# Performance work log

Measured on AMD Instinct MI355X. Metric: run time of the kernel, lower is better.

Reference implementation:

```python
import jax, jax.numpy as jnp
import numpy as np

N0, N1, N2 = 100000, 20000, 4000
DEG = 10
G_NODES = 200000
D, ED, CD, FF, NHEAD = 512, 256, 300, 2048, 2


def _layernorm(x, g, b, eps=1e-5):
    m = jnp.mean(x, -1, keepdims=True)
    v = jnp.var(x, -1, keepdims=True)
    return (x - m) * jax.lax.rsqrt(v + eps) * g + b


def _mha(q_in, kv_in, w_in, b_in, w_out, b_out):
    # torch nn.MultiheadAttention, inputs are (seq, batch, d)
    d = q_in.shape[-1]
    wq, wk, wv = w_in[:d], w_in[d:2 * d], w_in[2 * d:]
    bq, bk, bv = b_in[:d], b_in[d:2 * d], b_in[2 * d:]
    dh = d // NHEAD
    q = (q_in @ wq.T + bq).reshape(q_in.shape[0], q_in.shape[1], NHEAD, dh)
    k = (kv_in @ wk.T + bk).reshape(kv_in.shape[0], kv_in.shape[1], NHEAD, dh)
    v = (kv_in @ wv.T + bv).reshape(kv_in.shape[0], kv_in.shape[1], NHEAD, dh)
    scores = jnp.einsum('qnhd,knhd->nhqk', q, k) * (dh ** -0.5)
    o = jnp.einsum('nhqk,knhd->qnhd', jax.nn.softmax(scores, -1), v)
    o = o.reshape(q_in.shape[0], q_in.shape[1], d)
    return o @ w_out.T + b_out


def setup_inputs() -> dict:
    key = jax.random.key(0)
    k = lambda i: jax.random.fold_in(key, i)
    inp = {}
    inp['nid0'] = jax.random.randint(k(0), (N0,), 0, G_NODES, dtype=jnp.int32)
    inp['nid1'] = jax.random.randint(k(1), (N1,), 0, G_NODES, dtype=jnp.int32)
    inp['nid2'] = jax.random.randint(k(2), (N2,), 0, G_NODES, dtype=jnp.int32)
    inp['esrc0'] = jax.random.randint(k(3), (N1 * DEG,), 0, N0, dtype=jnp.int32)
    inp['edst0'] = jnp.repeat(jnp.arange(N1, dtype=jnp.int32), DEG)
    inp['esrc1'] = jax.random.randint(k(4), (N2 * DEG,), 0, N1, dtype=jnp.int32)
    inp['edst1'] = jnp.repeat(jnp.arange(N2, dtype=jnp.int32), DEG)
    inp['content0'] = jax.random.normal(k(5), (N0, CD), jnp.float32)
    inp['content1'] = jax.random.normal(k(6), (N1, CD), jnp.float32)
    inp['content2'] = jax.random.normal(k(7), (N2, CD), jnp.float32)
    inp['node_emb_w'] = jax.random.normal(k(8), (G_NODES + 1, ED), jnp.float32) / ED
    inp['ee_w'] = jax.random.normal(k(9), (D, ED), jnp.float32) * 0.06
    inp['ee_b'] = jax.random.normal(k(10), (D,), jnp.float32) * 0.001
    inp['proj_w'] = jax.random.normal(k(11), (D, CD), jnp.float32) * 0.06
    inp['proj_b'] = jax.random.normal(k(12), (D,), jnp.float32) * 0.001
    inp['proj_g'] = jnp.ones((D,), jnp.float32)
    inp['proj_beta'] = jnp.zeros((D,), jnp.float32)
    L = 2  # decoder layers
    inp['sa_in_w'] = jax.random.normal(k(13), (L, 3 * D, D), jnp.float32) * 0.04
    inp['sa_in_b'] = jnp.zeros((L, 3 * D), jnp.float32)
    inp['sa_out_w'] = jax.random.normal(k(14), (L, D, D), jnp.float32) * 0.04
    inp['sa_out_b'] = jnp.zeros((L, D), jnp.float32)
    inp['ca_in_w'] = jax.random.normal(k(15), (L, 3 * D, D), jnp.float32) * 0.04
    inp['ca_in_b'] = jnp.zeros((L, 3 * D), jnp.float32)
    inp['ca_out_w'] = jax.random.normal(k(16), (L, D, D), jnp.float32) * 0.04
    inp['ca_out_b'] = jnp.zeros((L, D), jnp.float32)
    inp['lin1_w'] = jax.random.normal(k(17), (L, FF, D), jnp.float32) * 0.03
    inp['lin1_b'] = jnp.zeros((L, FF), jnp.float32)
    inp['lin2_w'] = jax.random.normal(k(18), (L, D, FF), jnp.float32) * 0.03
    inp['lin2_b'] = jnp.zeros((L, D), jnp.float32)
    for n in ('n1', 'n2', 'n3'):
        inp[n + '_g'] = jnp.ones((L, D), jnp.float32)
        inp[n + '_b'] = jnp.zeros((L, D), jnp.float32)
    return inp


def _forward(nid0, nid1, nid2, esrc0, edst0, esrc1, edst1,
             content0, content1, content2, node_emb_w, ee_w, ee_b,
             proj_w, proj_b, proj_g, proj_beta,
             sa_in_w, sa_in_b, sa_out_w, sa_out_b,
             ca_in_w, ca_in_b, ca_out_w, ca_out_b,
             lin1_w, lin1_b, lin2_w, lin2_b,
             n1_g, n1_b, n2_g, n2_b, n3_g, n3_b):
    def node_h(nid, content):
        nh = node_emb_w[nid + 1] @ ee_w.T + ee_b           # emb_expand(node_emb(nid+1))
        c = _layernorm(jax.nn.leaky_relu(content @ proj_w.T + proj_b, 0.1), proj_g, proj_beta)
        h = nh + c                                          # mix_embeddings (c[:, :D] == c)
        return h / jnp.maximum(jnp.linalg.norm(h, axis=1, keepdims=True), 1e-5)

    h0 = node_h(nid0, content0)
    h1 = node_h(nid1, content1)
    h2 = node_h(nid2, content2)

    def agg_mean(h_src, src, dst, n_dst):
        s = jax.ops.segment_sum(h_src[src], dst, num_segments=n_dst)
        w = jax.ops.segment_sum(jnp.ones(src.shape[0], h_src.dtype), dst, num_segments=n_dst)
        return s / w[:, None]

    # block 0: non-prediction GraphConv -> concat(mean_agg, h), L2 normalize
    m1 = agg_mean(h0, esrc0, edst0, N1)
    h1 = jnp.concatenate([m1, h1], axis=1)                  # (N1, 2D)
    h1 = h1 / jnp.maximum(jnp.linalg.norm(h1, axis=1, keepdims=True), 1e-5)

    # block 1: prediction GraphConv -> transformer-decoder fusion
    m2 = agg_mean(h1, esrc1, edst1, N2)                     # (N2, 2D)
    mem = m2.reshape(N2, 2, D).transpose(1, 0, 2)           # (n_layer=2, N2, D)
    tgt = h2[None]                                          # (1, N2, D)
    for l in range(2):  # post-norm TransformerDecoderLayer, gelu, dropout=0
        t2 = _mha(tgt, tgt, sa_in_w[l], sa_in_b[l], sa_out_w[l], sa_out_b[l])
        tgt = _layernorm(tgt + t2, n1_g[l], n1_b[l])
        t2 = _mha(tgt, mem, ca_in_w[l], ca_in_b[l], ca_out_w[l], ca_out_b[l])
        tgt = _layernorm(tgt + t2, n2_g[l], n2_b[l])
        ff = jax.nn.gelu(tgt @ lin1_w[l].T + lin1_b[l], approximate=False) @ lin2_w[l].T + lin2_b[l]
        tgt = _layernorm(tgt + ff, n3_g[l], n3_b[l])
    out = tgt[0]                                            # squeeze -> (N2, D)
    return out / jnp.maximum(jnp.linalg.norm(out, axis=1, keepdims=True), 1e-5)


def reference(nid0, nid1, nid2, esrc0, edst0, esrc1, edst1,
              content0, content1, content2, node_emb_w, ee_w, ee_b,
              proj_w, proj_b, proj_g, proj_beta,
              sa_in_w, sa_in_b, sa_out_w, sa_out_b,
              ca_in_w, ca_in_b, ca_out_w, ca_out_b,
              lin1_w, lin1_b, lin2_w, lin2_b,
              n1_g, n1_b, n2_g, n2_b, n3_g, n3_b):
    return _forward(nid0, nid1, nid2, esrc0, edst0, esrc1, edst1,
                    content0, content1, content2, node_emb_w, ee_w, ee_b,
                    proj_w, proj_b, proj_g, proj_beta,
                    sa_in_w, sa_in_b, sa_out_w, sa_out_b,
                    ca_in_w, ca_in_b, ca_out_w, ca_out_b,
                    lin1_w, lin1_b, lin2_w, lin2_b,
                    n1_g, n1_b, n2_g, n2_b, n3_g, n3_b)
```

## Files before the change

kernel.cpp:

```cpp
#include <hip/hip_runtime.h>
#include <math.h>

static constexpr int kN0  = 100000;
static constexpr int kN1  = 20000;
static constexpr int kN2  = 4000;
static constexpr int kDeg = 10;
static constexpr int kD   = 512;
static constexpr int kFF  = 2048;
static constexpr int kRows  = 48;
static constexpr int kRowsN = 32;
static constexpr int kLdA  = 584;
static constexpr int kLdG  = 520;

using short8  = __attribute__((ext_vector_type(8))) short;
using floatx4 = __attribute__((ext_vector_type(4))) float;

__device__ inline unsigned short f2bf(float f) {
    union { float f; unsigned u; } v; v.f = f;
    unsigned r = v.u + 0x7FFFu + ((v.u >> 16) & 1u);
    return (unsigned short)(r >> 16);
}

__global__ __launch_bounds__(256) void pack_node_w_kernel(
    const float* __restrict__ ee_w, const float* __restrict__ proj_w,
    ushort* __restrict__ Bp)
{
    int tid  = blockIdx.x * 256 + threadIdx.x;
    int lane = tid & 63;
    int tile = tid >> 6;
    int n     = (tile & 31) * 16 + (lane & 15);
    int kbase = (tile >> 5) * 32 + (lane >> 4) * 8;
    ushort v[8];
    #pragma unroll
    for (int j = 0; j < 8; ++j) {
        int k = kbase + j;
        float f = 0.f;
        if (k < 256)      f = ee_w[(size_t)n * 256 + k];
        else if (k < 556) f = proj_w[(size_t)n * 300 + (k - 256)];
        v[j] = f2bf(f);
    }
    uint4 u;
    u.x = (unsigned)v[0] | ((unsigned)v[1] << 16);
    u.y = (unsigned)v[2] | ((unsigned)v[3] << 16);
    u.z = (unsigned)v[4] | ((unsigned)v[5] << 16);
    u.w = (unsigned)v[6] | ((unsigned)v[7] << 16);
    *(uint4*)(Bp + (size_t)tid * 8) = u;
}

__global__ __launch_bounds__(256) void pack512_many_kernel(
    const float* __restrict__ sa_in_w, const float* __restrict__ sa_out_w,
    const float* __restrict__ ca_in_w, const float* __restrict__ ca_out_w,
    ushort* __restrict__ dst)
{
    int y = blockIdx.y, l = y / 6, m = y % 6;
    const float* W;
    switch (m) {
        case 0: W = sa_in_w  + (size_t)l * 3 * kD * kD + (size_t)2 * kD * kD; break;
        case 1: W = sa_out_w + (size_t)l * kD * kD; break;
        case 2: W = ca_in_w  + (size_t)l * 3 * kD * kD; break;
        case 3: W = ca_in_w  + (size_t)l * 3 * kD * kD + (size_t)kD * kD; break;
        case 4: W = ca_in_w  + (size_t)l * 3 * kD * kD + (size_t)2 * kD * kD; break;
        default:W = ca_out_w + (size_t)l * kD * kD; break;
    }
    int tid  = blockIdx.x * 256 + threadIdx.x;
    int lane = tid & 63;
    int tile = tid >> 6;
    int n  = (tile & 31) * 16 + (lane & 15);
    int kb = (tile >> 5) * 32 + (lane >> 4) * 8;
    const float* src = W + (size_t)n * 512 + kb;
    ushort v[8];
    #pragma unroll
    for (int j = 0; j < 8; ++j) v[j] = f2bf(src[j]);
    uint4 u;
    u.x = (unsigned)v[0] | ((unsigned)v[1] << 16);
    u.y = (unsigned)v[2] | ((unsigned)v[3] << 16);
    u.z = (unsigned)v[4] | ((unsigned)v[5] << 16);
    u.w = (unsigned)v[6] | ((unsigned)v[7] << 16);
    *(uint4*)(dst + (size_t)y * 262144 + (size_t)tid * 8) = u;
}

__global__ __launch_bounds__(256) void pack_generic_kernel(
    const float* __restrict__ src, size_t srcStride,
    ushort* __restrict__ dst, size_t dstStride, int N, int K)
{
    int tid  = blockIdx.x * 256 + threadIdx.x;
    int NT = N >> 4;
    int lane = tid & 63;
    int tile = tid >> 6;
    int ct = tile % NT, kc = tile / NT;
    int n  = ct * 16 + (lane & 15);
    int kb = kc * 32 + (lane >> 4) * 8;
    const float* W = src + blockIdx.y * srcStride + (size_t)n * K + kb;
    ushort v[8];
    #pragma unroll
    for (int j = 0; j < 8; ++j) v[j] = f2bf(W[j]);
    uint4 u;
    u.x = (unsigned)v[0] | ((unsigned)v[1] << 16);
    u.y = (unsigned)v[2] | ((unsigned)v[3] << 16);
    u.z = (unsigned)v[4] | ((unsigned)v[5] << 16);
    u.w = (unsigned)v[6] | ((unsigned)v[7] << 16);
    *(uint4*)(dst + blockIdx.y * dstStride + (size_t)tid * 8) = u;
}

__global__ __launch_bounds__(512, 4) void node_h_mfma(
    const int* __restrict__ nid,
    const float* __restrict__ content,
    const float* __restrict__ node_emb_w,
    const ushort* __restrict__ Bp,
    const float* __restrict__ ee_b, const float* __restrict__ proj_b,
    const float* __restrict__ proj_g, const float* __restrict__ proj_beta,
    float* __restrict__ hout, int ldh, int n)
{
    __shared__ __align__(16) ushort As[kRowsN * kLdA];
    __shared__ float redS[8][kRowsN], redQ[8][kRowsN];
    __shared__ float meanv[kRowsN], rstdv[kRowsN], rowinv[kRowsN];

    const int t    = threadIdx.x;
    const int lane = t & 63;
    const int wv   = t >> 6;
    const int quad = lane >> 4;
    const int l15  = lane & 15;
    const int row0 = blockIdx.x * kRowsN;

    #pragma unroll
    for (int it = 0; it < 9; ++it) {
        int flat = it * 512 + t;
        int r  = flat / 144;
        int k4 = flat - r * 144;
        int row = row0 + r; if (row >= n) row = n - 1;
        float4 f = make_float4(0.f, 0.f, 0.f, 0.f);
        if (k4 < 64)
            f = *(const float4*)(node_emb_w + ((size_t)(nid[row] + 1)) * 256 + k4 * 4);
        else if (k4 < 139)
            f = *(const float4*)(content + (size_t)row * 300 + (k4 - 64) * 4);
        ushort4 o = make_ushort4(f2bf(f.x), f2bf(f.y), f2bf(f.z), f2bf(f.w));
        *(ushort4*)(As + (size_t)r * kLdA + k4 * 4) = o;
    }
    __syncthreads();

    floatx4 acc[2][4] = {};
    const short8* BpV = (const short8*)Bp;

    #pragma unroll
    for (int kc = 8; kc < 18; ++kc) {
        const short8* bp = BpV + (size_t)(kc * 32 + wv * 4) * 64 + lane;
        short8 b0 = bp[0], b1 = bp[64], b2 = bp[128], b3 = bp[192];
        short8 a[2];
        #pragma unroll
        for (int rt = 0; rt < 2; ++rt)
            a[rt] = *(const short8*)(As + (size_t)(rt * 16 + l15) * kLdA + kc * 32 + quad * 8);
        #pragma unroll
        for (int rt = 0; rt < 2; ++rt) {
            acc[rt][0] = __builtin_amdgcn_mfma_f32_16x16x32_bf16(a[rt], b0, acc[rt][0], 0, 0, 0);
            acc[rt][1] = __builtin_amdgcn_mfma_f32_16x16x32_bf16(a[rt], b1, acc[rt][1], 0, 0, 0);
            acc[rt][2] = __builtin_amdgcn_mfma_f32_16x16x32_bf16(a[rt], b2, acc[rt][2], 0, 0, 0);
            acc[rt][3] = __builtin_amdgcn_mfma_f32_16x16x32_bf16(a[rt], b3, acc[rt][3], 0, 0, 0);
        }
    }

    const int colbase = wv * 64 + l15;
    float pb[4], pg[4], pbt[4], eb[4];
    #pragma unroll
    for (int ct = 0; ct < 4; ++ct) {
        int c = colbase + ct * 16;
        pb[ct]  = proj_b[c];
        pg[ct]  = proj_g[c];
        pbt[ct] = proj_beta[c];
        eb[ct]  = ee_b[c];
    }

    float s8[8], q8[8];
    #pragma unroll
    for (int rt = 0; rt < 2; ++rt) {
        #pragma unroll
        for (int i = 0; i < 4; ++i) {
            float s = 0.f, q = 0.f;
            #pragma unroll
            for (int ct = 0; ct < 4; ++ct) {
                float c = acc[rt][ct][i] + pb[ct];
                c = (c >= 0.f) ? c : 0.1f * c;
                acc[rt][ct][i] = c;
                s += c; q = fmaf(c, c, q);
            }
            s8[rt * 4 + i] = s; q8[rt * 4 + i] = q;
        }
    }
    #pragma unroll
    for (int idx = 0; idx < 8; ++idx) {
        #pragma unroll
        for (int m = 1; m < 16; m <<= 1) {
            s8[idx] += __shfl_xor(s8[idx], m);
            q8[idx] += __shfl_xor(q8[idx], m);
        }
    }
    if (l15 == 0) {
        #pragma unroll
        for (int rt = 0; rt < 2; ++rt)
            #pragma unroll
            for (int i = 0; i < 4; ++i) {
                int rl = rt * 16 + quad * 4 + i;
                redS[wv][rl] = s8[rt * 4 + i];
                redQ[wv][rl] = q8[rt * 4 + i];
            }
    }
    __syncthreads();
    if (t < kRowsN) {
        float s = 0.f, q = 0.f;
        #pragma unroll
        for (int w = 0; w < 8; ++w) { s += redS[w][t]; q += redQ[w][t]; }
        float m   = s * (1.f / 512.f);
        float var = q * (1.f / 512.f) - m * m;
        meanv[t] = m;
        rstdv[t] = rsqrtf(var + 1e-5f);
    }
    __syncthreads();

    #pragma unroll
    for (int rt = 0; rt < 2; ++rt) {
        #pragma unroll
        for (int i = 0; i < 4; ++i) {
            int rl = rt * 16 + quad * 4 + i;
            float m = meanv[rl], rs = rstdv[rl];
            #pragma unroll
            for (int ct = 0; ct < 4; ++ct)
                acc[rt][ct][i] = (acc[rt][ct][i] - m) * rs * pg[ct] + pbt[ct] + eb[ct];
        }
    }

    #pragma unroll
    for (int kc = 0; kc < 8; ++kc) {
        const short8* bp = BpV + (size_t)(kc * 32 + wv * 4) * 64 + lane;
        short8 b0 = bp[0], b1 = bp[64], b2 = bp[128], b3 = bp[192];
        short8 a[2];
        #pragma unroll
        for (int rt = 0; rt < 2; ++rt)
            a[rt] = *(const short8*)(As + (size_t)(rt * 16 + l15) * kLdA + kc * 32 + quad * 8);
        #pragma unroll
        for (int rt = 0; rt < 2; ++rt) {
            acc[rt][0] = __builtin_amdgcn_mfma_f32_16x16x32_bf16(a[rt], b0, acc[rt][0], 0, 0, 0);
            acc[rt][1] = __builtin_amdgcn_mfma_f32_16x16x32_bf16(a[rt], b1, acc[rt][1], 0, 0, 0);
            acc[rt][2] = __builtin_amdgcn_mfma_f32_16x16x32_bf16(a[rt], b2, acc[rt][2], 0, 0, 0);
            acc[rt][3] = __builtin_amdgcn_mfma_f32_16x16x32_bf16(a[rt], b3, acc[rt][3], 0, 0, 0);
        }
    }

    #pragma unroll
    for (int rt = 0; rt < 2; ++rt) {
        #pragma unroll
        for (int i = 0; i < 4; ++i) {
            float psq = 0.f;
            #pragma unroll
            for (int ct = 0; ct < 4; ++ct)
                psq = fmaf(acc[rt][ct][i], acc[rt][ct][i], psq);
            q8[rt * 4 + i] = psq;
        }
    }
    #pragma unroll
    for (int idx = 0; idx < 8; ++idx)
        #pragma unroll
        for (int m = 1; m < 16; m <<= 1)
            q8[idx] += __shfl_xor(q8[idx], m);
    if (l15 == 0) {
        #pragma unroll
        for (int rt = 0; rt < 2; ++rt)
            #pragma unroll
            for (int i = 0; i < 4; ++i)
                redS[wv][rt * 16 + quad * 4 + i] = q8[rt * 4 + i];
    }
    __syncthreads();
    if (t < kRowsN) {
        float s = 0.f;
        #pragma unroll
        for (int w = 0; w < 8; ++w) s += redS[w][t];
        rowinv[t] = 1.f / fmaxf(sqrtf(s), 1e-5f);
    }
    __syncthreads();

    #pragma unroll
    for (int rt = 0; rt < 2; ++rt) {
        #pragma unroll
        for (int i = 0; i < 4; ++i) {
            int rl = rt * 16 + quad * 4 + i;
            int grow = row0 + rl;
            if (grow < n) {
                float inv = rowinv[rl];
                float* dst = hout + (size_t)grow * ldh + colbase;
                #pragma unroll
                for (int ct = 0; ct < 4; ++ct)
                    dst[ct * 16] = acc[rt][ct][i] * inv;
            }
        }
    }
}

__device__ inline float gelu_exact(float x) {
    return 0.5f * x * (1.f + erff(x * 0.70710678118654752f));
}

template<int EPI>
__global__ __launch_bounds__(512, 2) void gemm_mfma(
    const float* __restrict__ A, int lda,
    const ushort* __restrict__ Bp, const float* __restrict__ bias,
    float* __restrict__ C, int ldc,
    const float* __restrict__ resid,
    const float* __restrict__ lng, const float* __restrict__ lnb,
    int M, int K, int N)
{
    __shared__ __align__(16) ushort As[kRows * kLdG];
    __shared__ float redS[8][kRows], redQ[8][kRows];
    __shared__ float meanv[kRows], rstdv[kRows];

    const int t    = threadIdx.x;
    const int lane = t & 63;
    const int wv   = t >> 6;
    const int quad = lane >> 4;
    const int l15  = lane & 15;
    const int row0 = blockIdx.x * kRows;
    const int nb   = blockIdx.y;
    const int NT   = N >> 4;

    floatx4 acc[3][4] = {};
    const short8* BpV = (const short8*)Bp;

    for (int k0 = 0; k0 < K; k0 += 512) {
        #pragma unroll
        for (int it = 0; it < 12; ++it) {
            int flat = it * 512 + t;
            int r  = flat >> 7;
            int k4 = flat & 127;
            int row = row0 + r; if (row >= M) row = M - 1;
            float4 f = *(const float4*)(A + (size_t)row * lda + k0 + k4 * 4);
            ushort4 o = make_ushort4(f2bf(f.x), f2bf(f.y), f2bf(f.z), f2bf(f.w));
            *(ushort4*)(As + (size_t)r * kLdG + k4 * 4) = o;
        }
        __syncthreads();
        const int g0 = k0 >> 5;
        #pragma unroll
        for (int kc = 0; kc < 16; ++kc) {
            const short8* bp = BpV + ((size_t)(g0 + kc) * NT + nb * 32 + wv * 4) * 64 + lane;
            short8 b0 = bp[0], b1 = bp[64], b2 = bp[128], b3 = bp[192];
            short8 a[3];
            #pragma unroll
            for (int rt = 0; rt < 3; ++rt)
                a[rt] = *(const short8*)(As + (size_t)(rt * 16 + l15) * kLdG + kc * 32 + quad * 8);
            #pragma unroll
            for (int rt = 0; rt < 3; ++rt) {
                acc[rt][0] = __builtin_amdgcn_mfma_f32_16x16x32_bf16(a[rt], b0, acc[rt][0], 0, 0, 0);
                acc[rt][1] = __builtin_amdgcn_mfma_f32_16x16x32_bf16(a[rt], b1, acc[rt][1], 0, 0, 0);
                acc[rt][2] = __builtin_amdgcn_mfma_f32_16x16x32_bf16(a[rt], b2, acc[rt][2], 0, 0, 0);
                acc[rt][3] = __builtin_amdgcn_mfma_f32_16x16x32_bf16(a[rt], b3, acc[rt][3], 0, 0, 0);
            }
        }
        __syncthreads();
    }

    const int colloc = wv * 64 + l15;
    float b[4];
    #pragma unroll
    for (int ct = 0; ct < 4; ++ct) b[ct] = bias[nb * 512 + colloc + ct * 16];

    if constexpr (EPI == 0 || EPI == 1) {
        #pragma unroll
        for (int rt = 0; rt < 3; ++rt) {
            #pragma unroll
            for (int i = 0; i < 4; ++i) {
                int row = row0 + rt * 16 + quad * 4 + i;
                if (row < M) {
                    float* dst = C + (size_t)row * ldc + nb * 512 + colloc;
                    #pragma unroll
                    for (int ct = 0; ct < 4; ++ct) {
                        float v = acc[rt][ct][i] + b[ct];
                        if (EPI == 1) v = gelu_exact(v);
                        dst[ct * 16] = v;
                    }
                }
            }
        }
    } else {
        float lg[4], lb[4];
        #pragma unroll
        for (int ct = 0; ct < 4; ++ct) {
            lg[ct] = lng[colloc + ct * 16];
            lb[ct] = lnb[colloc + ct * 16];
        }
        float s12[12], q12[12];
        #pragma unroll
        for (int rt = 0; rt < 3; ++rt) {
            #pragma unroll
            for (int i = 0; i < 4; ++i) {
                int rl = rt * 16 + quad * 4 + i;
                int row = row0 + rl; if (row >= M) row = M - 1;
                const float* rr = resid + (size_t)row * 512 + colloc;
                float s = 0.f, q = 0.f;
                #pragma unroll
                for (int ct = 0; ct < 4; ++ct) {
                    float h = acc[rt][ct][i] + b[ct] + rr[ct * 16];
                    acc[rt][ct][i] = h;
                    s += h; q = fmaf(h, h, q);
                }
                s12[rt * 4 + i] = s; q12[rt * 4 + i] = q;
            }
        }
        #pragma unroll
        for (int idx = 0; idx < 12; ++idx) {
            #pragma unroll
            for (int m = 1; m < 16; m <<= 1) {
                s12[idx] += __shfl_xor(s12[idx], m);
                q12[idx] += __shfl_xor(q12[idx], m);
            }
        }
        if (l15 == 0) {
            #pragma unroll
            for (int rt = 0; rt < 3; ++rt)
                #pragma unroll
                for (int i = 0; i < 4; ++i) {
                    int rl = rt * 16 + quad * 4 + i;
                    redS[wv][rl] = s12[rt * 4 + i];
                    redQ[wv][rl] = q12[rt * 4 + i];
                }
        }
        __syncthreads();
        if (t < kRows) {
            float s = 0.f, q = 0.f;
            #pragma unroll
            for (int w = 0; w < 8; ++w) { s += redS[w][t]; q += redQ[w][t]; }
            float m   = s * (1.f / 512.f);
            float var = q * (1.f / 512.f) - m * m;
            meanv[t] = m;
            rstdv[t] = rsqrtf(var + 1e-5f);
        }
        __syncthreads();
        #pragma unroll
        for (int rt = 0; rt < 3; ++rt) {
            #pragma unroll
            for (int i = 0; i < 4; ++i) {
                int rl = rt * 16 + quad * 4 + i;
                int row = row0 + rl;
                if (row < M) {
                    float m = meanv[rl], rs = rstdv[rl];
                    float* dst = C + (size_t)row * 512 + colloc;
                    #pragma unroll
                    for (int ct = 0; ct < 4; ++ct)
                        dst[ct * 16] = (acc[rt][ct][i] - m) * rs * lg[ct] + lb[ct];
                }
            }
        }
    }
}

__device__ inline float block_sum256(float v, float* red4) {
    #pragma unroll
    for (int off = 32; off > 0; off >>= 1) v += __shfl_down(v, off);
    if ((threadIdx.x & 63) == 0) red4[threadIdx.x >> 6] = v;
    __syncthreads();
    return red4[0] + red4[1] + red4[2] + red4[3];
}

__global__ __launch_bounds__(256) void agg_norm1_kernel(
    const float* __restrict__ h0, const int* __restrict__ esrc,
    float* __restrict__ h1cat)
{
    __shared__ int idx[kDeg];
    __shared__ float red4[4];
    int i = blockIdx.x, t = threadIdx.x;
    if (t < kDeg) idx[t] = esrc[i * kDeg + t];
    __syncthreads();
    float s0 = 0.f, s1 = 0.f;
    for (int e = 0; e < kDeg; ++e) {
        const float* hr = h0 + (size_t)idx[e] * 512;
        s0 += hr[t]; s1 += hr[t + 256];
    }
    s0 *= 0.1f; s1 *= 0.1f;
    size_t base = (size_t)i * 1024;
    float o0 = h1cat[base + 512 + t];
    float o1 = h1cat[base + 768 + t];
    float tot = block_sum256(s0 * s0 + s1 * s1 + o0 * o0 + o1 * o1, red4);
    float inv = 1.f / fmaxf(sqrtf(tot), 1e-5f);
    h1cat[base + t]       = s0 * inv;
    h1cat[base + 256 + t] = s1 * inv;
    h1cat[base + 512 + t] = o0 * inv;
    h1cat[base + 768 + t] = o1 * inv;
}

__global__ __launch_bounds__(256) void agg2_kernel(
    const float* __restrict__ h1cat, const int* __restrict__ esrc,
    float* __restrict__ m2)
{
    __shared__ int idx[kDeg];
    int i = blockIdx.x, t = threadIdx.x;
    if (t < kDeg) idx[t] = esrc[i * kDeg + t];
    __syncthreads();
    float s0 = 0.f, s1 = 0.f, s2 = 0.f, s3 = 0.f;
    for (int e = 0; e < kDeg; ++e) {
        const float* hr = h1cat + (size_t)idx[e] * 1024;
        s0 += hr[t]; s1 += hr[t + 256]; s2 += hr[t + 512]; s3 += hr[t + 768];
    }
    size_t base = (size_t)i * 1024;
    m2[base + t]       = s0 * 0.1f;
    m2[base + 256 + t] = s1 * 0.1f;
    m2[base + 512 + t] = s2 * 0.1f;
    m2[base + 768 + t] = s3 * 0.1f;
}

__global__ __launch_bounds__(256) void attn_combine_kernel(
    const float* __restrict__ Q,
    const float* __restrict__ Kb, const float* __restrict__ Vb,
    float* __restrict__ O)
{
    __shared__ float red[4][4];
    __shared__ float a[4];
    int i = blockIdx.x, t = threadIdx.x;
    size_t base  = (size_t)i * 512;
    size_t base0 = (size_t)(2 * i) * 512;
    size_t base1 = base0 + 512;
    float q0 = Q[base + t], q1 = Q[base + t + 256];
    float p00 = q0 * Kb[base0 + t];
    float p01 = q0 * Kb[base1 + t];
    float p10 = q1 * Kb[base0 + t + 256];
    float p11 = q1 * Kb[base1 + t + 256];
    #pragma unroll
    for (int off = 32; off > 0; off >>= 1) {
        p00 += __shfl_down(p00, off);
        p01 += __shfl_down(p01, off);
        p10 += __shfl_down(p10, off);
        p11 += __shfl_down(p11, off);
    }
    int w = t >> 6;
    if ((t & 63) == 0) { red[w][0] = p00; red[w][1] = p01; red[w][2] = p10; red[w][3] = p11; }
    __syncthreads();
    if (t == 0) {
        float s00 = (red[0][0] + red[1][0] + red[2][0] + red[3][0]) * 0.0625f;
        float s01 = (red[0][1] + red[1][1] + red[2][1] + red[3][1]) * 0.0625f;
        float s10 = (red[0][2] + red[1][2] + red[2][2] + red[3][2]) * 0.0625f;
        float s11 = (red[0][3] + red[1][3] + red[2][3] + red[3][3]) * 0.0625f;
        float m0 = fmaxf(s00, s01);
        float e0 = expf(s00 - m0), e1 = expf(s01 - m0);
        float d0 = e0 + e1;
        a[0] = e0 / d0; a[1] = e1 / d0;
        float m1 = fmaxf(s10, s11);
        float f0 = expf(s10 - m1), f1 = expf(s11 - m1);
        float d1 = f0 + f1;
        a[2] = f0 / d1; a[3] = f1 / d1;
    }
    __syncthreads();
    O[base + t]       = a[0] * Vb[base0 + t]       + a[1] * Vb[base1 + t];
    O[base + t + 256] = a[2] * Vb[base0 + t + 256] + a[3] * Vb[base1 + t + 256];
}

__global__ __launch_bounds__(256) void final_norm_kernel(
    const float* __restrict__ tgt, float* __restrict__ out)
{
    __shared__ float red4[4];
    int i = blockIdx.x, t = threadIdx.x;
    size_t base = (size_t)i * 512;
    float v0 = tgt[base + t], v1 = tgt[base + t + 256];
    float tot = block_sum256(v0 * v0 + v1 * v1, red4);
    float inv = 1.f / fmaxf(sqrtf(tot), 1e-5f);
    out[base + t]       = v0 * inv;
    out[base + t + 256] = v1 * inv;
}

extern "C" void kernel_launch(void* const* d_in, const int* in_sizes, int n_in,
                              void* d_out, int out_size, void* d_ws, size_t ws_size,
                              hipStream_t stream)
{
    (void)in_sizes; (void)n_in; (void)out_size; (void)ws_size;
    const int*   nid0       = (const int*)d_in[0];
    const int*   nid1       = (const int*)d_in[1];
    const int*   nid2       = (const int*)d_in[2];
    const int*   esrc0      = (const int*)d_in[3];
    const int*   esrc1      = (const int*)d_in[5];
    const float* content0   = (const float*)d_in[7];
    const float* content1   = (const float*)d_in[8];
    const float* content2   = (const float*)d_in[9];
    const float* node_emb_w = (const float*)d_in[10];
    const float* ee_w       = (const float*)d_in[11];
    const float* ee_b       = (const float*)d_in[12];
    const float* proj_w     = (const float*)d_in[13];
    const float* proj_b     = (const float*)d_in[14];
    const float* proj_g     = (const float*)d_in[15];
    const float* proj_beta  = (const float*)d_in[16];
    const float* sa_in_w    = (const float*)d_in[17];
    const float* sa_in_b    = (const float*)d_in[18];
    const float* sa_out_w   = (const float*)d_in[19];
    const float* sa_out_b   = (const float*)d_in[20];
    const float* ca_in_w    = (const float*)d_in[21];
    const float* ca_in_b    = (const float*)d_in[22];
    const float* ca_out_w   = (const float*)d_in[23];
    const float* ca_out_b   = (const float*)d_in[24];
    const float* lin1_w     = (const float*)d_in[25];
    const float* lin1_b     = (const float*)d_in[26];
    const float* lin2_w     = (const float*)d_in[27];
    const float* lin2_b     = (const float*)d_in[28];
    const float* n1_g       = (const float*)d_in[29];
    const float* n1_b       = (const float*)d_in[30];
    const float* n2_g       = (const float*)d_in[31];
    const float* n2_b       = (const float*)d_in[32];
    const float* n3_g       = (const float*)d_in[33];
    const float* n3_b       = (const float*)d_in[34];

    float* ws = (float*)d_ws;
    size_t off = 0;
    float* h0    = ws + off; off += (size_t)kN0 * 512;
    float* h1cat = ws + off; off += (size_t)kN1 * 1024;
    float* m2    = ws + off; off += (size_t)kN2 * 1024;
    float* tgt   = ws + off; off += (size_t)kN2 * 512;
    float* Qb    = ws + off; off += (size_t)kN2 * 512;
    float* Kb    = ws + off; off += (size_t)2 * kN2 * 512;
    float* Vb    = ws + off; off += (size_t)2 * kN2 * 512;
    float* Ob    = ws + off; off += (size_t)kN2 * 512;
    float* ffh   = ws + off; off += (size_t)kN2 * 2048;
    ushort* BpNode = (ushort*)(ws + off); off += 147456;
    ushort* Pw512  = (ushort*)(ws + off); off += 12 * 262144 / 2;
    ushort* Pl1    = (ushort*)(ws + off); off += 2 * 1048576 / 2;
    ushort* Pl2    = (ushort*)(ws + off); off += 2 * 1048576 / 2;

    dim3 blk(256);

    pack_node_w_kernel<<<dim3(144), blk, 0, stream>>>(ee_w, proj_w, BpNode);
    pack512_many_kernel<<<dim3(128, 12), blk, 0, stream>>>(
        sa_in_w, sa_out_w, ca_in_w, ca_out_w, Pw512);
    pack_generic_kernel<<<dim3(512, 2), blk, 0, stream>>>(
        lin1_w, (size_t)kFF * kD, Pl1, 1048576, kFF, kD);
    pack_generic_kernel<<<dim3(512, 2), blk, 0, stream>>>(
        lin2_w, (size_t)kD * kFF, Pl2, 1048576, kD, kFF);

    node_h_mfma<<<dim3((kN0 + kRowsN - 1) / kRowsN), dim3(512), 0, stream>>>(
        nid0, content0, node_emb_w, BpNode, ee_b, proj_b, proj_g, proj_beta,
        h0, 512, kN0);
    node_h_mfma<<<dim3((kN1 + kRowsN - 1) / kRowsN), dim3(512), 0, stream>>>(
        nid1, content1, node_emb_w, BpNode, ee_b, proj_b, proj_g, proj_beta,
        h1cat + 512, 1024, kN1);
    node_h_mfma<<<dim3((kN2 + kRowsN - 1) / kRowsN), dim3(512), 0, stream>>>(
        nid2, content2, node_emb_w, BpNode, ee_b, proj_b, proj_g, proj_beta,
        tgt, 512, kN2);

    agg_norm1_kernel<<<dim3(kN1), blk, 0, stream>>>(h0, esrc0, h1cat);
    agg2_kernel<<<dim3(kN2), blk, 0, stream>>>(h1cat, esrc1, m2);

    const int M   = kN2;
    const int gM  = (M + kRows - 1) / kRows;
    const int gM2 = (2 * M + kRows - 1) / kRows;
    dim3 blk512(512);
    for (int l = 0; l < 2; ++l) {
        const ushort* sa_v_p   = Pw512 + (size_t)(l * 6 + 0) * 262144;
        const ushort* sa_out_p = Pw512 + (size_t)(l * 6 + 1) * 262144;
        const ushort* ca_q_p   = Pw512 + (size_t)(l * 6 + 2) * 262144;
        const ushort* ca_k_p   = Pw512 + (size_t)(l * 6 + 3) * 262144;
        const ushort* ca_v_p   = Pw512 + (size_t)(l * 6 + 4) * 262144;
        const ushort* ca_out_p = Pw512 + (size_t)(l * 6 + 5) * 262144;
        const ushort* l1_p     = Pl1 + (size_t)l * 1048576;
        const ushort* l2_p     = Pl2 + (size_t)l * 1048576;
        const float* sa_b = sa_in_b + (size_t)l * 3 * kD;
        const float* saob = sa_out_b + (size_t)l * kD;
        const float* ca_b = ca_in_b + (size_t)l * 3 * kD;
        const float* caob = ca_out_b + (size_t)l * kD;
        const float* l1b = lin1_b + (size_t)l * kFF;
        const float* l2b = lin2_b + (size_t)l * kD;

        gemm_mfma<0><<<dim3(gM, 1), blk512, 0, stream>>>(
            tgt, 512, sa_v_p, sa_b + 2 * kD, Qb, 512,
            nullptr, nullptr, nullptr, M, 512, 512);
        gemm_mfma<2><<<dim3(gM, 1), blk512, 0, stream>>>(
            Qb, 512, sa_out_p, saob, tgt, 512,
            tgt, n1_g + l * kD, n1_b + l * kD, M, 512, 512);

        gemm_mfma<0><<<dim3(gM, 1), blk512, 0, stream>>>(
            tgt, 512, ca_q_p, ca_b, Qb, 512,
            nullptr, nullptr, nullptr, M, 512, 512);
        gemm_mfma<0><<<dim3(gM2, 1), blk512, 0, stream>>>(
            m2, 512, ca_k_p, ca_b + kD, Kb, 512,
            nullptr, nullptr, nullptr, 2 * M, 512, 512);
        gemm_mfma<0><<<dim3(gM2, 1), blk512, 0, stream>>>(
            m2, 512, ca_v_p, ca_b + 2 * kD, Vb, 512,
            nullptr, nullptr, nullptr, 2 * M, 512, 512);
        attn_combine_kernel<<<dim3(M), blk, 0, stream>>>(Qb, Kb, Vb, Ob);
        gemm_mfma<2><<<dim3(gM, 1), blk512, 0, stream>>>(
            Ob, 512, ca_out_p, caob, tgt, 512,
            tgt, n2_g + l * kD, n2_b + l * kD, M, 512, 512);

        gemm_mfma<1><<<dim3(gM, 4), blk512, 0, stream>>>(
            tgt, 512, l1_p, l1b, ffh, 2048,
            nullptr, nullptr, nullptr, M, 512, 2048);
        gemm_mfma<2><<<dim3(gM, 1), blk512, 0, stream>>>(
            ffh, 2048, l2_p, l2b, tgt, 512,
            tgt, n3_g + l * kD, n3_b + l * kD, M, 2048, 512);
    }

    final_norm_kernel<<<dim3(kN2), blk, 0, stream>>>(tgt, (float*)d_out);
}
```

Baseline: 1.165 ms.

## Make node projection persistent with double-buffered prefetch; batch independent GEMM launches

The node_h_mfma kernel becomes a persistent kernel capped at 512 blocks. Each block loops over row groups, loading the next group's gathered embeddings and content into registers while the current group computes, then writing them to a second LDS buffer. Separately, the self-attention V projection and the cross-attention K/V projections are merged into one gemm3_mfma launch that picks its operands by block index. This trades more LDS and registers (which may lower occupancy) for overlapped loads and fewer launches.

```diff
diff --git a/kernel.cpp b/kernel.cpp
--- a/kernel.cpp
+++ b/kernel.cpp
@@ -109,9 +109,9 @@
     const ushort* __restrict__ Bp,
     const float* __restrict__ ee_b, const float* __restrict__ proj_b,
     const float* __restrict__ proj_g, const float* __restrict__ proj_beta,
-    float* __restrict__ hout, int ldh, int n)
-{
-    __shared__ __align__(16) ushort As[kRowsN * kLdA];
+    float* __restrict__ hout, int ldh, int n, int nGroups)
+{
+    __shared__ __align__(16) ushort As[2][kRowsN * kLdA];
     __shared__ float redS[8][kRowsN], redQ[8][kRowsN];
     __shared__ float meanv[kRowsN], rstdv[kRowsN], rowinv[kRowsN];
 
@@ -120,43 +120,7 @@
     const int wv   = t >> 6;
     const int quad = lane >> 4;
     const int l15  = lane & 15;
-    const int row0 = blockIdx.x * kRowsN;
-
-    #pragma unroll
-    for (int it = 0; it < 9; ++it) {
-        int flat = it * 512 + t;
-        int r  = flat / 144;
-        int k4 = flat - r * 144;
-        int row = row0 + r; if (row >= n) row = n - 1;
-        float4 f = make_float4(0.f, 0.f, 0.f, 0.f);
-        if (k4 < 64)
-            f = *(const float4*)(node_emb_w + ((size_t)(nid[row] + 1)) * 256 + k4 * 4);
-        else if (k4 < 139)
-            f = *(const float4*)(content + (size_t)row * 300 + (k4 - 64) * 4);
-        ushort4 o = make_ushort4(f2bf(f.x), f2bf(f.y), f2bf(f.z), f2bf(f.w));
-        *(ushort4*)(As + (size_t)r * kLdA + k4 * 4) = o;
-    }
-    __syncthreads();
-
-    floatx4 acc[2][4] = {};
-    const short8* BpV = (const short8*)Bp;
-
-    #pragma unroll
-    for (int kc = 8; kc < 18; ++kc) {
-        const short8* bp = BpV + (size_t)(kc * 32 + wv * 4) * 64 + lane;
-        short8 b0 = bp[0], b1 = bp[64], b2 = bp[128], b3 = bp[192];
-        short8 a[2];
-        #pragma unroll
-        for (int rt = 0; rt < 2; ++rt)
-            a[rt] = *(const short8*)(As + (size_t)(rt * 16 + l15) * kLdA + kc * 32 + quad * 8);
-        #pragma unroll
-        for (int rt = 0; rt < 2; ++rt) {
-            acc[rt][0] = __builtin_amdgcn_mfma_f32_16x16x32_bf16(a[rt], b0, acc[rt][0], 0, 0, 0);
-            acc[rt][1] = __builtin_amdgcn_mfma_f32_16x16x32_bf16(a[rt], b1, acc[rt][1], 0, 0, 0);
-            acc[rt][2] = __builtin_amdgcn_mfma_f32_16x16x32_bf16(a[rt], b2, acc[rt][2], 0, 0, 0);
-            acc[rt][3] = __builtin_amdgcn_mfma_f32_16x16x32_bf16(a[rt], b3, acc[rt][3], 0, 0, 0);
-        }
-    }
+    const int gStride = gridDim.x;
 
     const int colbase = wv * 64 + l15;
     float pb[4], pg[4], pbt[4], eb[4];
@@ -169,127 +133,199 @@
         eb[ct]  = ee_b[c];
     }
 
-    float s8[8], q8[8];
-    #pragma unroll
-    for (int rt = 0; rt < 2; ++rt) {
-        #pragma unroll
-        for (int i = 0; i < 4; ++i) {
+    float4 stg[9];
+
+    auto issue = [&](int g) {
+        int row0 = g * kRowsN;
+        #pragma unroll
+        for (int it = 0; it < 9; ++it) {
+            int flat = it * 512 + t;
+            int r  = flat / 144;
+            int k4 = flat - r * 144;
+            int row = row0 + r; if (row >= n) row = n - 1;
+            float4 f = make_float4(0.f, 0.f, 0.f, 0.f);
+            if (k4 < 64)
+                f = *(const float4*)(node_emb_w + (size_t)(nid[row] + 1) * 256 + (size_t)k4 * 4);
+            else if (k4 < 139)
+                f = *(const float4*)(content + (size_t)row * 300 + (size_t)(k4 - 64) * 4);
+            stg[it] = f;
+        }
+    };
+    auto flush = [&](ushort* dstAs) {
+        #pragma unroll
+        for (int it = 0; it < 9; ++it) {
+            int flat = it * 512 + t;
+            int r  = flat / 144;
+            int k4 = flat - r * 144;
+            float4 f = stg[it];
+            ushort4 o = make_ushort4(f2bf(f.x), f2bf(f.y), f2bf(f.z), f2bf(f.w));
+            *(ushort4*)(dstAs + (size_t)r * kLdA + k4 * 4) = o;
+        }
+    };
+
+    int g = blockIdx.x;
+    if (g >= nGroups) return;
+    issue(g);
+    flush(As[0]);
+    __syncthreads();
+    int cur = 0;
+    const short8* BpV = (const short8*)Bp;
+
+    while (true) {
+        const ushort* as = As[cur];
+        const int row0 = g * kRowsN;
+        const int gn = g + gStride;
+        const bool more = gn < nGroups;
+
+        floatx4 acc[2][4] = {};
+
+        #pragma unroll
+        for (int kc = 8; kc < 18; ++kc) {
+            const short8* bp = BpV + (size_t)(kc * 32 + wv * 4) * 64 + lane;
+            short8 b0 = bp[0], b1 = bp[64], b2 = bp[128], b3 = bp[192];
+            short8 a[2];
+            #pragma unroll
+            for (int rt = 0; rt < 2; ++rt)
+                a[rt] = *(const short8*)(as + (size_t)(rt * 16 + l15) * kLdA + kc * 32 + quad * 8);
+            #pragma unroll
+            for (int rt = 0; rt < 2; ++rt) {
+                acc[rt][0] = __builtin_amdgcn_mfma_f32_16x16x32_bf16(a[rt], b0, acc[rt][0], 0, 0, 0);
+                acc[rt][1] = __builtin_amdgcn_mfma_f32_16x16x32_bf16(a[rt], b1, acc[rt][1], 0, 0, 0);
+                acc[rt][2] = __builtin_amdgcn_mfma_f32_16x16x32_bf16(a[rt], b2, acc[rt][2], 0, 0, 0);
+                acc[rt][3] = __builtin_amdgcn_mfma_f32_16x16x32_bf16(a[rt], b3, acc[rt][3], 0, 0, 0);
+            }
+        }
+
+        if (more) issue(gn);
+
+        float s8[8], q8[8];
+        #pragma unroll
+        for (int rt = 0; rt < 2; ++rt) {
+            #pragma unroll
+            for (int i = 0; i < 4; ++i) {
+                float s = 0.f, q = 0.f;
+                #pragma unroll
+                for (int ct = 0; ct < 4; ++ct) {
+                    float c = acc[rt][ct][i] + pb[ct];
+                    c = (c >= 0.f) ? c : 0.1f * c;
+                    acc[rt][ct][i] = c;
+                    s += c; q = fmaf(c, c, q);
+                }
+                s8[rt * 4 + i] = s; q8[rt * 4 + i] = q;
+            }
+        }
+        #pragma unroll
+        for (int idx = 0; idx < 8; ++idx) {
+            #pragma unroll
+            for (int m = 1; m < 16; m <<= 1) {
+                s8[idx] += __shfl_xor(s8[idx], m);
+                q8[idx] += __shfl_xor(q8[idx], m);
+            }
+        }
+        if (l15 == 0) {
+            #pragma unroll
+            for (int rt = 0; rt < 2; ++rt)
+                #pragma unroll
+                for (int i = 0; i < 4; ++i) {
+                    int rl = rt * 16 + quad * 4 + i;
+                    redS[wv][rl] = s8[rt * 4 + i];
+                    redQ[wv][rl] = q8[rt * 4 + i];
+                }
+        }
+        __syncthreads();
+        if (t < kRowsN) {
             float s = 0.f, q = 0.f;
             #pragma unroll
-            for (int ct = 0; ct < 4; ++ct) {
-                float c = acc[rt][ct][i] + pb[ct];
-                c = (c >= 0.f) ? c : 0.1f * c;
-                acc[rt][ct][i] = c;
-                s += c; q = fmaf(c, c, q);
-            }
-            s8[rt * 4 + i] = s; q8[rt * 4 + i] = q;
-        }
-    }
-    #pragma unroll
-    for (int idx = 0; idx < 8; ++idx) {
-        #pragma unroll
-        for (int m = 1; m < 16; m <<= 1) {
-            s8[idx] += __shfl_xor(s8[idx], m);
-            q8[idx] += __shfl_xor(q8[idx], m);
-        }
-    }
-    if (l15 == 0) {
-        #pragma unroll
-        for (int rt = 0; rt < 2; ++rt)
+            for (int w = 0; w < 8; ++w) { s += redS[w][t]; q += redQ[w][t]; }
+            float m   = s * (1.f / 512.f);
+            float var = q * (1.f / 512.f) - m * m;
+            meanv[t] = m;
+            rstdv[t] = rsqrtf(var + 1e-5f);
+        }
+        __syncthreads();
+
+        #pragma unroll
+        for (int rt = 0; rt < 2; ++rt) {
             #pragma unroll
             for (int i = 0; i < 4; ++i) {
                 int rl = rt * 16 + quad * 4 + i;
-                redS[wv][rl] = s8[rt * 4 + i];
-                redQ[wv][rl] = q8[rt * 4 + i];
-            }
-    }
-    __syncthreads();
-    if (t < kRowsN) {
-        float s = 0.f, q = 0.f;
-        #pragma unroll
-        for (int w = 0; w < 8; ++w) { s += redS[w][t]; q += redQ[w][t]; }
-        float m   = s * (1.f / 512.f);
-        float var = q * (1.f / 512.f) - m * m;
-        meanv[t] = m;
-        rstdv[t] = rsqrtf(var + 1e-5f);
-    }
-    __syncthreads();
-
-    #pragma unroll
-    for (int rt = 0; rt < 2; ++rt) {
-        #pragma unroll
-        for (int i = 0; i < 4; ++i) {
-            int rl = rt * 16 + quad * 4 + i;
-            float m = meanv[rl], rs = rstdv[rl];
-            #pragma unroll
-            for (int ct = 0; ct < 4; ++ct)
-                acc[rt][ct][i] = (acc[rt][ct][i] - m) * rs * pg[ct] + pbt[ct] + eb[ct];
-        }
-    }
-
-    #pragma unroll
-    for (int kc = 0; kc < 8; ++kc) {
-        const short8* bp = BpV + (size_t)(kc * 32 + wv * 4) * 64 + lane;
-        short8 b0 = bp[0], b1 = bp[64], b2 = bp[128], b3 = bp[192];
-        short8 a[2];
-        #pragma unroll
-        for (int rt = 0; rt < 2; ++rt)
-            a[rt] = *(const short8*)(As + (size_t)(rt * 16 + l15) * kLdA + kc * 32 + quad * 8);
-        #pragma unroll
-        for (int rt = 0; rt < 2; ++rt) {
-            acc[rt][0] = __builtin_amdgcn_mfma_f32_16x16x32_bf16(a[rt], b0, acc[rt][0], 0, 0, 0);
-            acc[rt][1] = __builtin_amdgcn_mfma_f32_16x16x32_bf16(a[rt], b1, acc[rt][1], 0, 0, 0);
-            acc[rt][2] = __builtin_amdgcn_mfma_f32_16x16x32_bf16(a[rt], b2, acc[rt][2], 0, 0, 0);
-            acc[rt][3] = __builtin_amdgcn_mfma_f32_16x16x32_bf16(a[rt], b3, acc[rt][3], 0, 0, 0);
-        }
-    }
-
-    #pragma unroll
-    for (int rt = 0; rt < 2; ++rt) {
-        #pragma unroll
-        for (int i = 0; i < 4; ++i) {
-            float psq = 0.f;
-            #pragma unroll
-            for (int ct = 0; ct < 4; ++ct)
-                psq = fmaf(acc[rt][ct][i], acc[rt][ct][i], psq);
-            q8[rt * 4 + i] = psq;
-        }
-    }
-    #pragma unroll
-    for (int idx = 0; idx < 8; ++idx)
-        #pragma unroll
-        for (int m = 1; m < 16; m <<= 1)
-            q8[idx] += __shfl_xor(q8[idx], m);
-    if (l15 == 0) {
-        #pragma unroll
-        for (int rt = 0; rt < 2; ++rt)
-            #pragma unroll
-            for (int i = 0; i < 4; ++i)
-                redS[wv][rt * 16 + quad * 4 + i] = q8[rt * 4 + i];
-    }
-    __syncthreads();
-    if (t < kRowsN) {
-        float s = 0.f;
-        #pragma unroll
-        for (int w = 0; w < 8; ++w) s += redS[w][t];
-        rowinv[t] = 1.f / fmaxf(sqrtf(s), 1e-5f);
-    }
-    __syncthreads();
-
-    #pragma unroll
-    for (int rt = 0; rt < 2; ++rt) {
-        #pragma unroll
-        for (int i = 0; i < 4; ++i) {
-            int rl = rt * 16 + quad * 4 + i;
-            int grow = row0 + rl;
-            if (grow < n) {
-                float inv = rowinv[rl];
-                float* dst = hout + (size_t)grow * ldh + colbase;
+                float m = meanv[rl], rs = rstdv[rl];
                 #pragma unroll
                 for (int ct = 0; ct < 4; ++ct)
-                    dst[ct * 16] = acc[rt][ct][i] * inv;
-            }
-        }
+                    acc[rt][ct][i] = (acc[rt][ct][i] - m) * rs * pg[ct] + pbt[ct] + eb[ct];
+            }
+        }
+
+        #pragma unroll
+        for (int kc = 0; kc < 8; ++kc) {
+            const short8* bp = BpV + (size_t)(kc * 32 + wv * 4) * 64 + lane;
+            short8 b0 = bp[0], b1 = bp[64], b2 = bp[128], b3 = bp[192];
+            short8 a[2];
+            #pragma unroll
+            for (int rt = 0; rt < 2; ++rt)
+                a[rt] = *(const short8*)(as + (size_t)(rt * 16 + l15) * kLdA + kc * 32 + quad * 8);
+            #pragma unroll
+            for (int rt = 0; rt < 2; ++rt) {
+                acc[rt][0] = __builtin_amdgcn_mfma_f32_16x16x32_bf16(a[rt], b0, acc[rt][0], 0, 0, 0);
+                acc[rt][1] = __builtin_amdgcn_mfma_f32_16x16x32_bf16(a[rt], b1, acc[rt][1], 0, 0, 0);
+                acc[rt][2] = __builtin_amdgcn_mfma_f32_16x16x32_bf16(a[rt], b2, acc[rt][2], 0, 0, 0);
+                acc[rt][3] = __builtin_amdgcn_mfma_f32_16x16x32_bf16(a[rt], b3, acc[rt][3], 0, 0, 0);
+            }
+        }
+
+        #pragma unroll
+        for (int rt = 0; rt < 2; ++rt) {
+            #pragma unroll
+            for (int i = 0; i < 4; ++i) {
+                float psq = 0.f;
+                #pragma unroll
+                for (int ct = 0; ct < 4; ++ct)
+                    psq = fmaf(acc[rt][ct][i], acc[rt][ct][i], psq);
+                q8[rt * 4 + i] = psq;
+            }
+        }
+        #pragma unroll
+        for (int idx = 0; idx < 8; ++idx)
+            #pragma unroll
+            for (int m = 1; m < 16; m <<= 1)
+                q8[idx] += __shfl_xor(q8[idx], m);
+        if (l15 == 0) {
+            #pragma unroll
+            for (int rt = 0; rt < 2; ++rt)
+                #pragma unroll
+                for (int i = 0; i < 4; ++i)
+                    redS[wv][rt * 16 + quad * 4 + i] = q8[rt * 4 + i];
+        }
+        __syncthreads();
+        if (t < kRowsN) {
+            float s = 0.f;
+            #pragma unroll
+            for (int w = 0; w < 8; ++w) s += redS[w][t];
+            rowinv[t] = 1.f / fmaxf(sqrtf(s), 1e-5f);
+        }
+        __syncthreads();
+
+        #pragma unroll
+        for (int rt = 0; rt < 2; ++rt) {
+            #pragma unroll
+            for (int i = 0; i < 4; ++i) {
+                int rl = rt * 16 + quad * 4 + i;
+                int grow = row0 + rl;
+                if (grow < n) {
+                    float inv = rowinv[rl];
+                    float* dst = hout + (size_t)grow * ldh + colbase;
+                    #pragma unroll
+                    for (int ct = 0; ct < 4; ++ct)
+                        dst[ct * 16] = acc[rt][ct][i] * inv;
+                }
+            }
+        }
+
+        if (more) flush((ushort*)As[cur ^ 1]);
+        __syncthreads();
+        if (!more) break;
+        cur ^= 1;
+        g = gn;
     }
 }
 
@@ -443,6 +479,81 @@
                     for (int ct = 0; ct < 4; ++ct)
                         dst[ct * 16] = (acc[rt][ct][i] - m) * rs * lg[ct] + lb[ct];
                 }
+            }
+        }
+    }
+}
+
+__global__ __launch_bounds__(512, 2) void gemm3_mfma(
+    const float* __restrict__ A0, const ushort* __restrict__ B0,
+    const float* __restrict__ b0p, float* __restrict__ C0, int M0,
+    const float* __restrict__ A1, const ushort* __restrict__ B1,
+    const float* __restrict__ b1p, float* __restrict__ C1, int M1,
+    const float* __restrict__ A2, const ushort* __restrict__ B2,
+    const float* __restrict__ b2p, float* __restrict__ C2, int M2)
+{
+    __shared__ __align__(16) ushort As[kRows * kLdG];
+
+    const int t    = threadIdx.x;
+    const int lane = t & 63;
+    const int wv   = t >> 6;
+    const int quad = lane >> 4;
+    const int l15  = lane & 15;
+
+    const int g0 = (M0 + kRows - 1) / kRows;
+    const int g1 = (M1 + kRows - 1) / kRows;
+    int bx = blockIdx.x;
+    const float* A; const ushort* Bw; const float* bias; float* C; int M;
+    if (bx < g0)           { A = A0; Bw = B0; bias = b0p; C = C0; M = M0; }
+    else if (bx < g0 + g1) { bx -= g0; A = A1; Bw = B1; bias = b1p; C = C1; M = M1; }
+    else                   { bx -= g0 + g1; A = A2; Bw = B2; bias = b2p; C = C2; M = M2; }
+    const int row0 = bx * kRows;
+
+    floatx4 acc[3][4] = {};
+    const short8* BpV = (const short8*)Bw;
+
+    #pragma unroll
+    for (int it = 0; it < 12; ++it) {
+        int flat = it * 512 + t;
+        int r  = flat >> 7;
+        int k4 = flat & 127;
+        int row = row0 + r; if (row >= M) row = M - 1;
+        float4 f = *(const float4*)(A + (size_t)row * 512 + k4 * 4);
+        ushort4 o = make_ushort4(f2bf(f.x), f2bf(f.y), f2bf(f.z), f2bf(f.w));
+        *(ushort4*)(As + (size_t)r * kLdG + k4 * 4) = o;
+    }
+    __syncthreads();
+    #pragma unroll
+    for (int kc = 0; kc < 16; ++kc) {
+        const short8* bp = BpV + ((size_t)kc * 32 + wv * 4) * 64 + lane;
+        short8 b0 = bp[0], b1 = bp[64], b2 = bp[128], b3 = bp[192];
+        short8 a[3];
+        #pragma unroll
+        for (int rt = 0; rt < 3; ++rt)
+            a[rt] = *(const short8*)(As + (size_t)(rt * 16 + l15) * kLdG + kc * 32 + quad * 8);
+        #pragma unroll
+        for (int rt = 0; rt < 3; ++rt) {
+            acc[rt][0] = __builtin_amdgcn_mfma_f32_16x16x32_bf16(a[rt], b0, acc[rt][0], 0, 0, 0);
+            acc[rt][1] = __builtin_amdgcn_mfma_f32_16x16x32_bf16(a[rt], b1, acc[rt][1], 0, 0, 0);
+            acc[rt][2] = __builtin_amdgcn_mfma_f32_16x16x32_bf16(a[rt], b2, acc[rt][2], 0, 0, 0);
+            acc[rt][3] = __builtin_amdgcn_mfma_f32_16x16x32_bf16(a[rt], b3, acc[rt][3], 0, 0, 0);
+        }
+    }
+
+    const int colloc = wv * 64 + l15;
+    float b[4];
+    #pragma unroll
+    for (int ct = 0; ct < 4; ++ct) b[ct] = bias[colloc + ct * 16];
+    #pragma unroll
+    for (int rt = 0; rt < 3; ++rt) {
+        #pragma unroll
+        for (int i = 0; i < 4; ++i) {
+            int row = row0 + rt * 16 + quad * 4 + i;
+            if (row < M) {
+                float* dst = C + (size_t)row * 512 + colloc;
+                #pragma unroll
+                for (int ct = 0; ct < 4; ++ct)
+                    dst[ct * 16] = acc[rt][ct][i] + b[ct];
             }
         }
     }
@@ -625,15 +736,23 @@
     pack_generic_kernel<<<dim3(512, 2), blk, 0, stream>>>(
         lin2_w, (size_t)kD * kFF, Pl2, 1048576, kD, kFF);
 
-    node_h_mfma<<<dim3((kN0 + kRowsN - 1) / kRowsN), dim3(512), 0, stream>>>(
-        nid0, content0, node_emb_w, BpNode, ee_b, proj_b, proj_g, proj_beta,
-        h0, 512, kN0);
-    node_h_mfma<<<dim3((kN1 + kRowsN - 1) / kRowsN), dim3(512), 0, stream>>>(
-        nid1, content1, node_emb_w, BpNode, ee_b, proj_b, proj_g, proj_beta,
-        h1cat + 512, 1024, kN1);
-    node_h_mfma<<<dim3((kN2 + kRowsN - 1) / kRowsN), dim3(512), 0, stream>>>(
-        nid2, content2, node_emb_w, BpNode, ee_b, proj_b, proj_g, proj_beta,
-        tgt, 512, kN2);
+    {
+        int grp0 = (kN0 + kRowsN - 1) / kRowsN;
+        int grp1 = (kN1 + kRowsN - 1) / kRowsN;
+        int grp2 = (kN2 + kRowsN - 1) / kRowsN;
+        int g0 = grp0 < 512 ? grp0 : 512;
+        int g1 = grp1 < 512 ? grp1 : 512;
+        int g2 = grp2 < 512 ? grp2 : 512;
+        node_h_mfma<<<dim3(g0), dim3(512), 0, stream>>>(
+            nid0, content0, node_emb_w, BpNode, ee_b, proj_b, proj_g, proj_beta,
+            h0, 512, kN0, grp0);
+        node_h_mfma<<<dim3(g1), dim3(512), 0, stream>>>(
+            nid1, content1, node_emb_w, BpNode, ee_b, proj_b, proj_g, proj_beta,
+            h1cat + 512, 1024, kN1, grp1);
+        node_h_mfma<<<dim3(g2), dim3(512), 0, stream>>>(
+            nid2, content2, node_emb_w, BpNode, ee_b, proj_b, proj_g, proj_beta,
+            tgt, 512, kN2, grp2);
+    }
 
     agg_norm1_kernel<<<dim3(kN1), blk, 0, stream>>>(h0, esrc0, h1cat);
     agg2_kernel<<<dim3(kN2), blk, 0, stream>>>(h1cat, esrc1, m2);
@@ -658,9 +777,11 @@
         const float* l1b = lin1_b + (size_t)l * kFF;
         const float* l2b = lin2_b + (size_t)l * kD;
 
-        gemm_mfma<0><<<dim3(gM, 1), blk512, 0, stream>>>(
-            tgt, 512, sa_v_p, sa_b + 2 * kD, Qb, 512,
-            nullptr, nullptr, nullptr, M, 512, 512);
+        gemm3_mfma<<<dim3(gM + gM2 + gM2), blk512, 0, stream>>>(
+            tgt, sa_v_p, sa_b + 2 * kD, Qb, M,
+            m2,  ca_k_p, ca_b + kD,     Kb, 2 * M,
+            m2,  ca_v_p, ca_b + 2 * kD, Vb, 2 * M);
+
         gemm_mfma<2><<<dim3(gM, 1), blk512, 0, stream>>>(
             Qb, 512, sa_out_p, saob, tgt, 512,
             tgt, n1_g + l * kD, n1_b + l * kD, M, 512, 512);
@@ -668,12 +789,6 @@
         gemm_mfma<0><<<dim3(gM, 1), blk512, 0, stream>>>(
             tgt, 512, ca_q_p, ca_b, Qb, 512,
             nullptr, nullptr, nullptr, M, 512, 512);
-        gemm_mfma<0><<<dim3(gM2, 1), blk512, 0, stream>>>(
-            m2, 512, ca_k_p, ca_b + kD, Kb, 512,
-            nullptr, nullptr, nullptr, 2 * M, 512, 512);
-        gemm_mfma<0><<<dim3(gM2, 1), blk512, 0, stream>>>(
-            m2, 512, ca_v_p, ca_b + 2 * kD, Vb, 512,
-            nullptr, nullptr, nullptr, 2 * M, 512, 512);
         attn_combine_kernel<<<dim3(M), blk, 0, stream>>>(Qb, Kb, Vb, Ob);
         gemm_mfma<2><<<dim3(gM, 1), blk512, 0, stream>>>(
             Ob, 512, ca_out_p, caob, tgt, 512,
```

Result: slower. 2.118 ms (+81.7%).
